# Kernel tuning notes

Measured on AMD Instinct MI355X. Metric: run time of the kernel, lower is better.

Reference implementation:

```python
import jax, jax.numpy as jnp
import numpy as np

B, N, C, H, DEPTH, MLP = 8, 1024, 768, 12, 8, 3072
HD = C // H
SCALE = HD ** -0.5
EPS = 1e-5


def layer_norm(x, g, b):
    mu = jnp.mean(x, -1, keepdims=True)
    var = jnp.mean((x - mu) ** 2, -1, keepdims=True)
    return (x - mu) / jnp.sqrt(var + EPS) * g + b


def setup_inputs() -> dict:
    key = jax.random.key(0)
    ks = jax.random.split(key, 8)
    s = 0.02
    return {
        "x": jax.random.normal(ks[0], (B, N, C), jnp.float32),
        "ln1_g": jnp.ones((DEPTH, C), jnp.float32),
        "ln1_b": jnp.zeros((DEPTH, C), jnp.float32),
        "wqkv": jax.random.normal(ks[1], (DEPTH, C, 3 * C), jnp.float32) * s,
        "wproj": jax.random.normal(ks[2], (DEPTH, C, C), jnp.float32) * s,
        "bproj": jnp.zeros((DEPTH, C), jnp.float32),
        "ln2_g": jnp.ones((DEPTH, C), jnp.float32),
        "ln2_b": jnp.zeros((DEPTH, C), jnp.float32),
        "w1": jax.random.normal(ks[3], (DEPTH, C, MLP), jnp.float32) * s,
        "b1": jnp.zeros((DEPTH, MLP), jnp.float32),
        "w2": jax.random.normal(ks[4], (DEPTH, MLP, C), jnp.float32) * s,
        "b2": jnp.zeros((DEPTH, C), jnp.float32),
    }


def reference(x, ln1_g, ln1_b, wqkv, wproj, bproj, ln2_g, ln2_b, w1, b1, w2, b2):
    def body(h, p):
        g1, be1, wq, wp, bp, g2, be2, wf1, bf1, wf2, bf2 = p
        # --- attention block: Residual(PreNorm(SelfAttention)) ---
        y = layer_norm(h, g1, be1)
        qkv = (y @ wq).reshape(B, N, 3, H, HD)
        qkv = jnp.transpose(qkv, (2, 0, 3, 1, 4))  # [3, B, H, N, HD]
        q, k, v = qkv[0], qkv[1], qkv[2]
        logits = jnp.einsum("bhnd,bhmd->bhnm", q, k) * SCALE
        # source applies softmax twice (faithful to original)
        attn = jax.nn.softmax(jax.nn.softmax(logits, axis=-1), axis=-1)
        o = jnp.einsum("bhnm,bhmd->bhnd", attn, v)
        o = jnp.transpose(o, (0, 2, 1, 3)).reshape(B, N, C)
        h = h + o @ wp + bp
        # --- FFN block: Residual(PreNorm(FeedForward)) ---
        y2 = layer_norm(h, g2, be2)
        f = jax.nn.relu(y2 @ wf1 + bf1) @ wf2 + bf2
        return h + f, None

    out, _ = jax.lax.scan(body, x, (ln1_g, ln1_b, wqkv, wproj, bproj, ln2_g, ln2_b, w1, b1, w2, b2))
    return out
```

## Files before the change

### kernel.cpp

```cpp
#include <hip/hip_runtime.h>
#include <hip/hip_bf16.h>

#define DEPTHL 8
#define BZ 8
#define SEQ 1024
#define CDIM 768
#define HEADS 12
#define HDIM 64
#define MLPD 3072
#define TOK (BZ*SEQ)
#define QKVN (3*CDIM)

typedef __attribute__((ext_vector_type(8))) short vshort8;
typedef __attribute__((ext_vector_type(4))) short vshort4;
typedef __attribute__((ext_vector_type(4))) float vfloat4;

__device__ __forceinline__ short bf16_bits(float f) {
  union { float f; unsigned u; } x; x.f = f;
  unsigned r = (x.u + 0x7FFFu + ((x.u >> 16) & 1u)) >> 16;
  return (short)r;
}

__device__ __forceinline__ unsigned pk_bf16(float a, float b) {
  unsigned r;
  asm("v_cvt_pk_bf16_f32 %0, %1, %2" : "=v"(r) : "v"(a), "v"(b));
  return r;
}

#define GL16(g, l) __builtin_amdgcn_global_load_lds( \
    (const __attribute__((address_space(1))) unsigned int*)(g), \
    (__attribute__((address_space(3))) unsigned int*)(l), 16, 0, 0)

__global__ __launch_bounds__(256) void wconv_t(const float* __restrict__ in,
                                               short* __restrict__ out,
                                               int K, int N) {
  __shared__ float tile[32][33];
  const long d = blockIdx.z;
  in  += d * (long)K * N;
  out += d * (long)N * K;
  const int n0 = blockIdx.x * 32, k0 = blockIdx.y * 32;
  const int tx = threadIdx.x & 31, ty = threadIdx.x >> 5;
#pragma unroll
  for (int i = 0; i < 4; i++)
    tile[ty + 8*i][tx] = in[(long)(k0 + ty + 8*i) * N + n0 + tx];
  __syncthreads();
#pragma unroll
  for (int i = 0; i < 4; i++)
    out[(long)(n0 + ty + 8*i) * K + k0 + tx] = bf16_bits(tile[tx][ty + 8*i]);
}

__global__ __launch_bounds__(256) void vtrans(const short* __restrict__ qkv,
                                              short* __restrict__ vt) {
  __shared__ short tile[32][34];
  const int bh = blockIdx.z;
  const int b = bh / HEADS, hh = bh % HEADS;
  const int t0 = blockIdx.x * 32, d0 = blockIdx.y * 32;
  const int tx = threadIdx.x & 31, ty = threadIdx.x >> 5;
  const short* src = qkv + ((long)b * SEQ + t0) * QKVN + 2 * CDIM + hh * HDIM + d0;
#pragma unroll
  for (int i = 0; i < 4; i++)
    tile[ty + 8*i][tx] = src[(long)(ty + 8*i) * QKVN + tx];
  __syncthreads();
  short* dst = vt + (long)bh * HDIM * SEQ + (long)d0 * SEQ + t0;
#pragma unroll
  for (int i = 0; i < 4; i++)
    dst[(long)(ty + 8*i) * SEQ + tx] = tile[tx][ty + 8*i];
}

__global__ __launch_bounds__(256) void ln_fwd(const float* __restrict__ h,
                                              const float* __restrict__ g,
                                              const float* __restrict__ be,
                                              short* __restrict__ y) {
  const int row = blockIdx.x * 4 + (threadIdx.x >> 6);
  const int lane = threadIdx.x & 63;
  const float4* hr = (const float4*)(h + (long)row * CDIM);
  const float4 v0 = hr[lane], v1 = hr[lane + 64], v2 = hr[lane + 128];
  float s = (v0.x + v0.y + v0.z + v0.w) + (v1.x + v1.y + v1.z + v1.w)
          + (v2.x + v2.y + v2.z + v2.w);
#pragma unroll
  for (int m = 32; m >= 1; m >>= 1) s += __shfl_xor(s, m);
  const float mu = s * (1.0f / CDIM);
  float d0x = v0.x - mu, d0y = v0.y - mu, d0z = v0.z - mu, d0w = v0.w - mu;
  float d1x = v1.x - mu, d1y = v1.y - mu, d1z = v1.z - mu, d1w = v1.w - mu;
  float d2x = v2.x - mu, d2y = v2.y - mu, d2z = v2.z - mu, d2w = v2.w - mu;
  float q = (d0x*d0x + d0y*d0y + d0z*d0z + d0w*d0w)
          + (d1x*d1x + d1y*d1y + d1z*d1z + d1w*d1w)
          + (d2x*d2x + d2y*d2y + d2z*d2z + d2w*d2w);
#pragma unroll
  for (int m = 32; m >= 1; m >>= 1) q += __shfl_xor(q, m);
  const float rstd = rsqrtf(q * (1.0f / CDIM) + 1e-5f);
  const float4* gp = (const float4*)g;
  const float4* bp = (const float4*)be;
  short* yr = y + (long)row * CDIM;
#pragma unroll
  for (int c = 0; c < 3; c++) {
    const float4 g4 = gp[lane + c * 64];
    const float4 b4 = bp[lane + c * 64];
    float dx = (c == 0 ? d0x : c == 1 ? d1x : d2x);
    float dy = (c == 0 ? d0y : c == 1 ? d1y : d2y);
    float dz = (c == 0 ? d0z : c == 1 ? d1z : d2z);
    float dw = (c == 0 ? d0w : c == 1 ? d1w : d2w);
    vshort4 o;
    o[0] = bf16_bits(dx * rstd * g4.x + b4.x);
    o[1] = bf16_bits(dy * rstd * g4.y + b4.y);
    o[2] = bf16_bits(dz * rstd * g4.z + b4.z);
    o[3] = bf16_bits(dw * rstd * g4.w + b4.w);
    *(vshort4*)(yr + c * 256 + lane * 4) = o;
  }
}

template<int EPI>
__global__ __launch_bounds__(256) void gemm_bt(const short* __restrict__ A,
                                               const short* __restrict__ Bt,
                                               const float* __restrict__ bias,
                                               void* __restrict__ Cout,
                                               int M, int N, int K) {
  __shared__ short As[128 * 64];
  __shared__ short Bs[128 * 64];
  const int tid = threadIdx.x;
  const int wid = tid >> 6, lane = tid & 63;
  const int lg = lane >> 4, lr = lane & 15;
  const int wm = wid >> 1, wn = wid & 1;

  const int gx = gridDim.x;
  const int nwg = gx * gridDim.y;
  int flat = blockIdx.y * gx + blockIdx.x;
  flat = (flat & 7) * (nwg >> 3) + (flat >> 3);
  const long bx = flat % gx;
  const long by = flat / gx;

  vfloat4 acc[4][4];
#pragma unroll
  for (int i = 0; i < 4; i++)
#pragma unroll
    for (int j = 0; j < 4; j++) acc[i][j] = (vfloat4){0.f, 0.f, 0.f, 0.f};

  const short* Abase = A  + by * 128 * (long)K;
  const short* Bbase = Bt + bx * 128 * (long)K;

  for (int kk = 0; kk < K; kk += 64) {
    __syncthreads();
#pragma unroll
    for (int ch = 0; ch < 4; ch++) {
      const int dst = tid * 16 + ch * 4096;
      const int off = dst ^ (((dst >> 7) & 7) << 4);
      const long srow = off >> 7;
      const int scol = (off & 127) >> 1;
      GL16(Abase + srow * K + kk + scol, As + (dst >> 1));
      GL16(Bbase + srow * K + kk + scol, Bs + (dst >> 1));
    }
    __syncthreads();
#pragma unroll
    for (int kh = 0; kh < 2; kh++) {
      vshort8 a[4], b[4];
#pragma unroll
      for (int mt = 0; mt < 4; mt++) {
        const int row = wm * 64 + mt * 16 + lr;
        int byt = row * 128 + kh * 64 + lg * 16;
        byt ^= (row & 7) << 4;
        a[mt] = *(const vshort8*)((const char*)As + byt);
      }
#pragma unroll
      for (int nt = 0; nt < 4; nt++) {
        const int row = wn * 64 + nt * 16 + lr;
        int byt = row * 128 + kh * 64 + lg * 16;
        byt ^= (row & 7) << 4;
        b[nt] = *(const vshort8*)((const char*)Bs + byt);
      }
#pragma unroll
      for (int mt = 0; mt < 4; mt++)
#pragma unroll
        for (int nt = 0; nt < 4; nt++)
          acc[mt][nt] = __builtin_amdgcn_mfma_f32_16x16x32_bf16(a[mt], b[nt], acc[mt][nt], 0, 0, 0);
    }
  }

  const long row0 = by * 128 + wm * 64;
  const long col0 = bx * 128 + wn * 64;
#pragma unroll
  for (int mt = 0; mt < 4; mt++) {
#pragma unroll
    for (int nt = 0; nt < 4; nt++) {
      const long col = col0 + nt * 16 + lr;
      float bv = 0.f;
      if (EPI != 0) bv = bias[col];
#pragma unroll
      for (int r = 0; r < 4; r++) {
        const long row = row0 + mt * 16 + lg * 4 + r;
        float v = acc[mt][nt][r];
        if (EPI == 0) {
          ((short*)Cout)[row * N + col] = bf16_bits(v);
        } else if (EPI == 1) {
          v += bv; v = v > 0.f ? v : 0.f;
          ((short*)Cout)[row * N + col] = bf16_bits(v);
        } else {
          float* hp = (float*)Cout + row * N + col;
          *hp = *hp + v + bv;
        }
      }
    }
  }
}

__global__ __launch_bounds__(256) void attn_fused6(const short* __restrict__ qkv,
                                                   const short* __restrict__ vt,
                                                   short* __restrict__ o) {
  __shared__ __align__(16) short P_lds[4 * 2 * 4096];
  __shared__ float redm[4][16], redz[4][16], redt[4][16];
  int flat = blockIdx.y * 32 + blockIdx.x;
  flat = (flat & 7) * (3072 >> 3) + (flat >> 3);
  const int qt = flat & 31;
  const int bh = flat >> 5;
  const int b = bh / HEADS, hh = bh % HEADS;
  const int tid = threadIdx.x, wid = tid >> 6, lane = tid & 63;
  const int lg = lane >> 4, lr = lane & 15;
  const long tokbase = (long)b * SEQ;
  const short* qbase = qkv + tokbase * QKVN + hh * HDIM;
  const short* kbase = qkv + tokbase * QKVN + CDIM + hh * HDIM;
  const short* vtb = vt + (long)bh * HDIM * SEQ;
  char* Pw0 = (char*)P_lds + wid * 16384;
  char* Pw1 = Pw0 + 8192;

  vshort8 qf0[2], qf1[2];
#pragma unroll
  for (int ks = 0; ks < 2; ks++) {
    qf0[ks] = *(const vshort8*)(qbase + (long)(qt * 32 + lr) * QKVN + ks * 32 + lg * 8);
    qf1[ks] = *(const vshort8*)(qbase + (long)(qt * 32 + 16 + lr) * QKVN + ks * 32 + lg * 8);
  }

  vfloat4 s0[16], s1[16];
#pragma unroll
  for (int bb = 0; bb < 4; bb++) {
    vshort8 kf[8];
#pragma unroll
    for (int u = 0; u < 4; u++) {
      const int n0 = wid * 256 + (bb * 4 + u) * 16;
#pragma unroll
      for (int ks = 0; ks < 2; ks++)
        kf[u * 2 + ks] = *(const vshort8*)(kbase + (long)(n0 + lr) * QKVN + ks * 32 + lg * 8);
    }
#pragma unroll
    for (int u = 0; u < 4; u++) {
      vfloat4 a0 = (vfloat4){0.f, 0.f, 0.f, 0.f};
      a0 = __builtin_amdgcn_mfma_f32_16x16x32_bf16(kf[u * 2 + 0], qf0[0], a0, 0, 0, 0);
      a0 = __builtin_amdgcn_mfma_f32_16x16x32_bf16(kf[u * 2 + 1], qf0[1], a0, 0, 0, 0);
      s0[bb * 4 + u] = a0;
      vfloat4 a1 = (vfloat4){0.f, 0.f, 0.f, 0.f};
      a1 = __builtin_amdgcn_mfma_f32_16x16x32_bf16(kf[u * 2 + 0], qf1[0], a1, 0, 0, 0);
      a1 = __builtin_amdgcn_mfma_f32_16x16x32_bf16(kf[u * 2 + 1], qf1[1], a1, 0, 0, 0);
      s1[bb * 4 + u] = a1;
    }
  }

  float rt0, rt1;
#define SOFTMAX_HALF(S, RT)                                                   \
  {                                                                           \
    float mt16[16];                                                           \
    _Pragma("unroll")                                                         \
    for (int i = 0; i < 16; i++)                                              \
      mt16[i] = fmaxf(fmaxf(S[i][0], S[i][1]), fmaxf(S[i][2], S[i][3]));      \
    _Pragma("unroll")                                                         \
    for (int st = 8; st >= 1; st >>= 1)                                       \
      _Pragma("unroll")                                                       \
      for (int i = 0; i < 8; i++) if (i < st) mt16[i] = fmaxf(mt16[i], mt16[i + st]); \
    float m = mt16[0];                                                        \
    m = fmaxf(m, __shfl_xor(m, 16));                                          \
    m = fmaxf(m, __shfl_xor(m, 32));                                          \
    if (lane < 16) redm[wid][lr] = m;                                         \
    __syncthreads();                                                          \
    m = fmaxf(fmaxf(redm[0][lr], redm[1][lr]), fmaxf(redm[2][lr], redm[3][lr])); \
    const float msc = m * 0.125f;                                             \
    float zt[16];                                                             \
    _Pragma("unroll")                                                         \
    for (int i = 0; i < 16; i++) {                                            \
      float e0 = __expf(fmaf(S[i][0], 0.125f, -msc));                         \
      float e1 = __expf(fmaf(S[i][1], 0.125f, -msc));                         \
      float e2 = __expf(fmaf(S[i][2], 0.125f, -msc));                         \
      float e3 = __expf(fmaf(S[i][3], 0.125f, -msc));                         \
      S[i][0] = e0; S[i][1] = e1; S[i][2] = e2; S[i][3] = e3;                 \
      zt[i] = (e0 + e1) + (e2 + e3);                                          \
    }                                                                         \
    _Pragma("unroll")                                                         \
    for (int st = 8; st >= 1; st >>= 1)                                       \
      _Pragma("unroll")                                                       \
      for (int i = 0; i < 8; i++) if (i < st) zt[i] += zt[i + st];            \
    float z = zt[0];                                                          \
    z += __shfl_xor(z, 16);                                                   \
    z += __shfl_xor(z, 32);                                                   \
    if (lane < 16) redz[wid][lr] = z;                                         \
    __syncthreads();                                                          \
    z = (redz[0][lr] + redz[1][lr]) + (redz[2][lr] + redz[3][lr]);            \
    const float rz = 1.0f / z;                                                \
    float tt[16];                                                             \
    _Pragma("unroll")                                                         \
    for (int i = 0; i < 16; i++) {                                            \
      float p0 = __expf(S[i][0] * rz);                                        \
      float p1 = __expf(S[i][1] * rz);                                        \
      float p2 = __expf(S[i][2] * rz);                                        \
      float p3 = __expf(S[i][3] * rz);                                        \
      S[i][0] = p0; S[i][1] = p1; S[i][2] = p2; S[i][3] = p3;                 \
      tt[i] = (p0 + p1) + (p2 + p3);                                          \
    }                                                                         \
    _Pragma("unroll")                                                         \
    for (int st = 8; st >= 1; st >>= 1)                                       \
      _Pragma("unroll")                                                       \
      for (int i = 0; i < 8; i++) if (i < st) tt[i] += tt[i + st];            \
    float t2 = tt[0];                                                         \
    t2 += __shfl_xor(t2, 16);                                                 \
    t2 += __shfl_xor(t2, 32);                                                 \
    if (lane < 16) redt[wid][lr] = t2;                                        \
    __syncthreads();                                                          \
    t2 = (redt[0][lr] + redt[1][lr]) + (redt[2][lr] + redt[3][lr]);           \
    RT = 1.0f / t2;                                                           \
  }

  SOFTMAX_HALF(s0, rt0)
  SOFTMAX_HALF(s1, rt1)
#undef SOFTMAX_HALF

#pragma unroll
  for (int i = 0; i < 16; i++) {
    const int byt = (lr * 512 + i * 32 + lg * 8) ^ ((lr & 7) << 4);
    uint2 pk0, pk1;
    pk0.x = pk_bf16(s0[i][0] * rt0, s0[i][1] * rt0);
    pk0.y = pk_bf16(s0[i][2] * rt0, s0[i][3] * rt0);
    pk1.x = pk_bf16(s1[i][0] * rt1, s1[i][1] * rt1);
    pk1.y = pk_bf16(s1[i][2] * rt1, s1[i][3] * rt1);
    *(uint2*)(Pw0 + byt) = pk0;
    *(uint2*)(Pw1 + byt) = pk1;
  }

  vfloat4 o0[4], o1[4];
#pragma unroll
  for (int dt = 0; dt < 4; dt++) {
    o0[dt] = (vfloat4){0.f, 0.f, 0.f, 0.f};
    o1[dt] = (vfloat4){0.f, 0.f, 0.f, 0.f};
  }
#pragma unroll
  for (int j = 0; j < 8; j++) {
    const int abyt = (lr * 512 + j * 64 + lg * 16) ^ ((lr & 7) << 4);
    vshort8 af0 = *(const vshort8*)(Pw0 + abyt);
    vshort8 af1 = *(const vshort8*)(Pw1 + abyt);
#pragma unroll
    for (int dt = 0; dt < 4; dt++) {
      vshort8 vb = *(const vshort8*)(vtb + (long)(dt * 16 + lr) * SEQ + wid * 256 + j * 32 + lg * 8);
      o0[dt] = __builtin_amdgcn_mfma_f32_16x16x32_bf16(af0, vb, o0[dt], 0, 0, 0);
      o1[dt] = __builtin_amdgcn_mfma_f32_16x16x32_bf16(af1, vb, o1[dt], 0, 0, 0);
    }
  }

#pragma unroll
  for (int dt = 0; dt < 4; dt++)
#pragma unroll
    for (int r = 0; r < 4; r++) {
      *(float*)(Pw0 + ((lg * 4 + r) * 64 + dt * 16 + lr) * 4) = o0[dt][r];
      *(float*)(Pw1 + ((lg * 4 + r) * 64 + dt * 16 + lr) * 4) = o1[dt][r];
    }
  __syncthreads();

  const int q = tid >> 4, d0 = (tid & 15) * 4;
#pragma unroll
  for (int h = 0; h < 2; h++) {
    const int ro = h * 8192 + (q * 64 + d0) * 4;
    float4 a0 = *(const float4*)((const char*)P_lds + 0 * 16384 + ro);
    float4 a1 = *(const float4*)((const char*)P_lds + 1 * 16384 + ro);
    float4 a2 = *(const float4*)((const char*)P_lds + 2 * 16384 + ro);
    float4 a3 = *(const float4*)((const char*)P_lds + 3 * 16384 + ro);
    float ox = (a0.x + a1.x) + (a2.x + a3.x);
    float oy = (a0.y + a1.y) + (a2.y + a3.y);
    float oz = (a0.z + a1.z) + (a2.z + a3.z);
    float ow = (a0.w + a1.w) + (a2.w + a3.w);
    uint2 ob;
    ob.x = pk_bf16(ox, oy);
    ob.y = pk_bf16(oz, ow);
    *(uint2*)(o + (tokbase + qt * 32 + h * 16 + q) * CDIM + hh * HDIM + d0) = ob;
  }
}

extern "C" void kernel_launch(void* const* d_in, const int* in_sizes, int n_in,
                              void* d_out, int out_size, void* d_ws, size_t ws_size,
                              hipStream_t stream) {
  const float* x     = (const float*)d_in[0];
  const float* ln1_g = (const float*)d_in[1];
  const float* ln1_b = (const float*)d_in[2];
  const float* wqkv  = (const float*)d_in[3];
  const float* wproj = (const float*)d_in[4];
  const float* bproj = (const float*)d_in[5];
  const float* ln2_g = (const float*)d_in[6];
  const float* ln2_b = (const float*)d_in[7];
  const float* w1    = (const float*)d_in[8];
  const float* b1    = (const float*)d_in[9];
  const float* w2    = (const float*)d_in[10];
  const float* b2    = (const float*)d_in[11];
  float* h = (float*)d_out;

  char* ws = (char*)d_ws;
  short* wqkv_t  = (short*)ws; ws += (size_t)DEPTHL * QKVN * CDIM * 2;
  short* wproj_t = (short*)ws; ws += (size_t)DEPTHL * CDIM * CDIM * 2;
  short* w1_t    = (short*)ws; ws += (size_t)DEPTHL * MLPD * CDIM * 2;
  short* w2_t    = (short*)ws; ws += (size_t)DEPTHL * CDIM * MLPD * 2;
  short* ybf     = (short*)ws; ws += (size_t)TOK * CDIM * 2;
  short* qkvbf   = (short*)ws; ws += (size_t)TOK * QKVN * 2;
  short* obf     = (short*)ws; ws += (size_t)TOK * CDIM * 2;
  short* f1bf    = (short*)ws; ws += (size_t)TOK * MLPD * 2;
  short* vtb     = f1bf;

  hipMemcpyAsync(h, x, (size_t)TOK * CDIM * sizeof(float), hipMemcpyDeviceToDevice, stream);

  wconv_t<<<dim3(QKVN / 32, CDIM / 32, DEPTHL), 256, 0, stream>>>(wqkv, wqkv_t, CDIM, QKVN);
  wconv_t<<<dim3(CDIM / 32, CDIM / 32, DEPTHL), 256, 0, stream>>>(wproj, wproj_t, CDIM, CDIM);
  wconv_t<<<dim3(MLPD / 32, CDIM / 32, DEPTHL), 256, 0, stream>>>(w1, w1_t, CDIM, MLPD);
  wconv_t<<<dim3(CDIM / 32, MLPD / 32, DEPTHL), 256, 0, stream>>>(w2, w2_t, MLPD, CDIM);

  for (int l = 0; l < DEPTHL; l++) {
    ln_fwd<<<TOK / 4, 256, 0, stream>>>(h, ln1_g + l * CDIM, ln1_b + l * CDIM, ybf);
    gemm_bt<0><<<dim3(QKVN / 128, TOK / 128), 256, 0, stream>>>(
        ybf, wqkv_t + (size_t)l * QKVN * CDIM, nullptr, qkvbf, TOK, QKVN, CDIM);
    vtrans<<<dim3(SEQ / 32, HDIM / 32, BZ * HEADS), 256, 0, stream>>>(qkvbf, vtb);
    attn_fused6<<<dim3(SEQ / 32, BZ * HEADS), 256, 0, stream>>>(qkvbf, vtb, obf);
    gemm_bt<2><<<dim3(CDIM / 128, TOK / 128), 256, 0, stream>>>(
        obf, wproj_t + (size_t)l * CDIM * CDIM, bproj + l * CDIM, h, TOK, CDIM, CDIM);
    ln_fwd<<<TOK / 4, 256, 0, stream>>>(h, ln2_g + l * CDIM, ln2_b + l * CDIM, ybf);
    gemm_bt<1><<<dim3(MLPD / 128, TOK / 128), 256, 0, stream>>>(
        ybf, w1_t + (size_t)l * MLPD * CDIM, b1 + l * MLPD, f1bf, TOK, MLPD, CDIM);
    gemm_bt<2><<<dim3(CDIM / 128, TOK / 128), 256, 0, stream>>>(
        f1bf, w2_t + (size_t)l * CDIM * MLPD, b2 + l * CDIM, h, TOK, CDIM, MLPD);
  }
}
```

Baseline: 3.310 ms.

## Fuse V transpose into QKV GEMM epilogue and use larger-tile MLP-up GEMM

Measured after the change: 3.571 ms. 7.9% more time.

```diff
diff --git a/kernel.cpp b/kernel.cpp
--- a/kernel.cpp
+++ b/kernel.cpp
@@ -47,24 +47,6 @@
 #pragma unroll
   for (int i = 0; i < 4; i++)
     out[(long)(n0 + ty + 8*i) * K + k0 + tx] = bf16_bits(tile[tx][ty + 8*i]);
-}
-
-__global__ __launch_bounds__(256) void vtrans(const short* __restrict__ qkv,
-                                              short* __restrict__ vt) {
-  __shared__ short tile[32][34];
-  const int bh = blockIdx.z;
-  const int b = bh / HEADS, hh = bh % HEADS;
-  const int t0 = blockIdx.x * 32, d0 = blockIdx.y * 32;
-  const int tx = threadIdx.x & 31, ty = threadIdx.x >> 5;
-  const short* src = qkv + ((long)b * SEQ + t0) * QKVN + 2 * CDIM + hh * HDIM + d0;
-#pragma unroll
-  for (int i = 0; i < 4; i++)
-    tile[ty + 8*i][tx] = src[(long)(ty + 8*i) * QKVN + tx];
-  __syncthreads();
-  short* dst = vt + (long)bh * HDIM * SEQ + (long)d0 * SEQ + t0;
-#pragma unroll
-  for (int i = 0; i < 4; i++)
-    dst[(long)(ty + 8*i) * SEQ + tx] = tile[tx][ty + 8*i];
 }
 
 __global__ __launch_bounds__(256) void ln_fwd(const float* __restrict__ h,
@@ -114,6 +96,7 @@
                                                const short* __restrict__ Bt,
                                                const float* __restrict__ bias,
                                                void* __restrict__ Cout,
+                                               short* __restrict__ vt2,
                                                int M, int N, int K) {
   __shared__ short As[128 * 64];
   __shared__ short Bs[128 * 64];
@@ -181,6 +164,114 @@
   for (int mt = 0; mt < 4; mt++) {
 #pragma unroll
     for (int nt = 0; nt < 4; nt++) {
+      const long col = col0 + nt * 16 + lr;
+      float bv = 0.f;
+      if (EPI == 1 || EPI == 2) bv = bias[col];
+#pragma unroll
+      for (int r = 0; r < 4; r++) {
+        const long row = row0 + mt * 16 + lg * 4 + r;
+        float v = acc[mt][nt][r];
+        if (EPI == 0) {
+          ((short*)Cout)[row * N + col] = bf16_bits(v);
+        } else if (EPI == 1) {
+          v += bv; v = v > 0.f ? v : 0.f;
+          ((short*)Cout)[row * N + col] = bf16_bits(v);
+        } else if (EPI == 2) {
+          float* hp = (float*)Cout + row * N + col;
+          *hp = *hp + v + bv;
+        } else {
+          const short bb = bf16_bits(v);
+          ((short*)Cout)[row * N + col] = bb;
+          if (col >= 2 * CDIM) {
+            const int dg = (int)col - 2 * CDIM;
+            const int hh2 = dg >> 6, dd = dg & 63;
+            const long bidx = row >> 10, tok = row & 1023;
+            vt2[(((bidx * HEADS + hh2) << 6) + dd) * (long)SEQ + tok] = bb;
+          }
+        }
+      }
+    }
+  }
+}
+
+template<int EPI>
+__global__ __launch_bounds__(512) void gemm_mk(const short* __restrict__ A,
+                                               const short* __restrict__ Bt,
+                                               const float* __restrict__ bias,
+                                               void* __restrict__ Cout,
+                                               int M, int N, int K) {
+  __shared__ short As[256 * 64];
+  __shared__ short Bs[128 * 64];
+  const int tid = threadIdx.x;
+  const int wid = tid >> 6, lane = tid & 63;
+  const int lg = lane >> 4, lr = lane & 15;
+
+  const int gx = gridDim.x;
+  const int nwg = gx * gridDim.y;
+  int flat = blockIdx.y * gx + blockIdx.x;
+  flat = (flat & 7) * (nwg >> 3) + (flat >> 3);
+  const long bx = flat % gx;
+  const long by = flat / gx;
+
+  vfloat4 acc[2][8];
+#pragma unroll
+  for (int i = 0; i < 2; i++)
+#pragma unroll
+    for (int j = 0; j < 8; j++) acc[i][j] = (vfloat4){0.f, 0.f, 0.f, 0.f};
+
+  const short* Abase = A  + by * 256 * (long)K;
+  const short* Bbase = Bt + bx * 128 * (long)K;
+
+  for (int kk = 0; kk < K; kk += 64) {
+    __syncthreads();
+#pragma unroll
+    for (int ch = 0; ch < 4; ch++) {
+      const int dst = tid * 16 + ch * 8192;
+      const int off = dst ^ (((dst >> 7) & 7) << 4);
+      const long srow = off >> 7;
+      const int scol = (off & 127) >> 1;
+      GL16(Abase + srow * K + kk + scol, As + (dst >> 1));
+    }
+#pragma unroll
+    for (int ch = 0; ch < 2; ch++) {
+      const int dst = tid * 16 + ch * 8192;
+      const int off = dst ^ (((dst >> 7) & 7) << 4);
+      const long srow = off >> 7;
+      const int scol = (off & 127) >> 1;
+      GL16(Bbase + srow * K + kk + scol, Bs + (dst >> 1));
+    }
+    __syncthreads();
+#pragma unroll
+    for (int kh = 0; kh < 2; kh++) {
+      vshort8 a[2], b[8];
+#pragma unroll
+      for (int mt = 0; mt < 2; mt++) {
+        const int row = wid * 32 + mt * 16 + lr;
+        int byt = row * 128 + kh * 64 + lg * 16;
+        byt ^= (row & 7) << 4;
+        a[mt] = *(const vshort8*)((const char*)As + byt);
+      }
+#pragma unroll
+      for (int nt = 0; nt < 8; nt++) {
+        const int row = nt * 16 + lr;
+        int byt = row * 128 + kh * 64 + lg * 16;
+        byt ^= (row & 7) << 4;
+        b[nt] = *(const vshort8*)((const char*)Bs + byt);
+      }
+#pragma unroll
+      for (int mt = 0; mt < 2; mt++)
+#pragma unroll
+        for (int nt = 0; nt < 8; nt++)
+          acc[mt][nt] = __builtin_amdgcn_mfma_f32_16x16x32_bf16(a[mt], b[nt], acc[mt][nt], 0, 0, 0);
+    }
+  }
+
+  const long row0 = by * 256 + wid * 32;
+  const long col0 = bx * 128;
+#pragma unroll
+  for (int mt = 0; mt < 2; mt++) {
+#pragma unroll
+    for (int nt = 0; nt < 8; nt++) {
       const long col = col0 + nt * 16 + lr;
       float bv = 0.f;
       if (EPI != 0) bv = bias[col];
@@ -414,16 +505,15 @@
 
   for (int l = 0; l < DEPTHL; l++) {
     ln_fwd<<<TOK / 4, 256, 0, stream>>>(h, ln1_g + l * CDIM, ln1_b + l * CDIM, ybf);
-    gemm_bt<0><<<dim3(QKVN / 128, TOK / 128), 256, 0, stream>>>(
-        ybf, wqkv_t + (size_t)l * QKVN * CDIM, nullptr, qkvbf, TOK, QKVN, CDIM);
-    vtrans<<<dim3(SEQ / 32, HDIM / 32, BZ * HEADS), 256, 0, stream>>>(qkvbf, vtb);
+    gemm_bt<3><<<dim3(QKVN / 128, TOK / 128), 256, 0, stream>>>(
+        ybf, wqkv_t + (size_t)l * QKVN * CDIM, nullptr, qkvbf, vtb, TOK, QKVN, CDIM);
     attn_fused6<<<dim3(SEQ / 32, BZ * HEADS), 256, 0, stream>>>(qkvbf, vtb, obf);
     gemm_bt<2><<<dim3(CDIM / 128, TOK / 128), 256, 0, stream>>>(
-        obf, wproj_t + (size_t)l * CDIM * CDIM, bproj + l * CDIM, h, TOK, CDIM, CDIM);
+        obf, wproj_t + (size_t)l * CDIM * CDIM, bproj + l * CDIM, h, nullptr, TOK, CDIM, CDIM);
     ln_fwd<<<TOK / 4, 256, 0, stream>>>(h, ln2_g + l * CDIM, ln2_b + l * CDIM, ybf);
-    gemm_bt<1><<<dim3(MLPD / 128, TOK / 128), 256, 0, stream>>>(
+    gemm_mk<1><<<dim3(MLPD / 128, TOK / 256), 512, 0, stream>>>(
         ybf, w1_t + (size_t)l * MLPD * CDIM, b1 + l * MLPD, f1bf, TOK, MLPD, CDIM);
     gemm_bt<2><<<dim3(CDIM / 128, TOK / 128), 256, 0, stream>>>(
-        f1bf, w2_t + (size_t)l * CDIM * MLPD, b2 + l * CDIM, h, TOK, CDIM, MLPD);
-  }
-}
+        f1bf, w2_t + (size_t)l * CDIM * MLPD, b2 + l * CDIM, h, nullptr, TOK, CDIM, MLPD);
+  }
+}
```
